# Kernel optimization log

Measured on AMD Instinct MI355X. Metric: run time of the kernel, lower is better.

The kernel has to match this reference:

```python
import jax, jax.numpy as jnp
import numpy as np

N_PRO = 100000
N_LIG = 100000
E = 500000
H = 128
CE = 18


def _lin_params(key, out_dim, in_dim, scale=0.02):
    kw, kb = jax.random.split(key)
    W = jax.random.normal(kw, (out_dim, in_dim), jnp.float32) * scale
    b = jax.random.normal(kb, (out_dim,), jnp.float32) * scale
    return W, b


def setup_inputs() -> dict:
    key = jax.random.key(0)
    ks = jax.random.split(key, 16)
    inp = {}
    inp['pro_x'] = jax.random.normal(ks[0], (N_PRO, H), jnp.float32)
    inp['lig_x'] = jax.random.normal(ks[1], (N_LIG, H), jnp.float32)
    pi = jax.random.randint(ks[2], (E,), 0, N_PRO)
    li = jax.random.randint(ks[3], (E,), 0, N_LIG)
    inp['cross_ei'] = jnp.stack([pi, li]).astype(jnp.int64)
    inp['cross_ea'] = jax.random.normal(ks[4], (E, CE), jnp.float32)
    inp['Wq_pro'], inp['bq_pro'] = _lin_params(ks[5], H, H)
    inp['Wk_lig'], inp['bk_lig'] = _lin_params(ks[6], H, H)
    inp['Wv_lig'], inp['bv_lig'] = _lin_params(ks[7], H, H)
    inp['Wq_lig'], inp['bq_lig'] = _lin_params(ks[8], H, H)
    inp['Wk_pro'], inp['bk_pro'] = _lin_params(ks[9], H, H)
    inp['Wv_pro'], inp['bv_pro'] = _lin_params(ks[10], H, H)
    inp['We_bias'] = jax.random.normal(ks[11], (CE,), jnp.float32) * 0.02  # Linear(CE,1,bias=False) weight
    inp['Wo_pro'], inp['bo_pro'] = _lin_params(ks[12], H, H)
    inp['Wo_lig'], inp['bo_lig'] = _lin_params(ks[13], H, H)
    inp['g_pro'] = jnp.ones((H,), jnp.float32)
    inp['be_pro'] = jnp.zeros((H,), jnp.float32)
    inp['g_lig'] = jnp.ones((H,), jnp.float32)
    inp['be_lig'] = jnp.zeros((H,), jnp.float32)
    return inp


def _layernorm(x, g, b, eps=1e-5):
    mu = jnp.mean(x, -1, keepdims=True)
    var = jnp.var(x, -1, keepdims=True)
    return (x - mu) * jax.lax.rsqrt(var + eps) * g + b


def _lin(x, W, b):
    return x @ W.T + b


def _attend(Q_src, K_tgt, V_tgt, bias, tgt_idx, n_tgt, scale):
    # per-edge score -> edge softmax over target nodes -> weighted scatter-add
    scores = jnp.sum(Q_src * K_tgt, -1) * scale + bias          # [E]
    scores = scores - jnp.max(scores)                            # global max, as in torch code
    exp_s = jnp.exp(scores)
    denom = jax.ops.segment_sum(exp_s, tgt_idx, num_segments=n_tgt)
    w = exp_s / (denom[tgt_idx] + 1e-8)                          # [E]
    return jax.ops.segment_sum(w[:, None] * V_tgt, tgt_idx, num_segments=n_tgt)  # [n_tgt, H]


def reference(pro_x, lig_x, cross_ei, cross_ea,
              Wq_pro, bq_pro, Wk_lig, bk_lig, Wv_lig, bv_lig,
              Wq_lig, bq_lig, Wk_pro, bk_pro, Wv_pro, bv_pro,
              We_bias, Wo_pro, bo_pro, Wo_lig, bo_lig,
              g_pro, be_pro, g_lig, be_lig):
    pi = cross_ei[0]
    li = cross_ei[1]
    h = pro_x.shape[1]
    scale = h ** (-0.5)
    bias = cross_ea @ We_bias                                    # [E]

    # protein <- ligand
    Qp = _lin(pro_x, Wq_pro, bq_pro)[pi]
    Kl = _lin(lig_x, Wk_lig, bk_lig)[li]
    Vl = _lin(lig_x, Wv_lig, bv_lig)[li]
    pro_upd = _attend(Qp, Kl, Vl, bias, pi, pro_x.shape[0], scale)
    pro_new = _layernorm(pro_x + _lin(pro_upd, Wo_pro, bo_pro), g_pro, be_pro)

    # ligand <- protein
    Ql = _lin(lig_x, Wq_lig, bq_lig)[li]
    Kp = _lin(pro_x, Wk_pro, bk_pro)[pi]
    Vp = _lin(pro_x, Wv_pro, bv_pro)[pi]
    lig_upd = _attend(Ql, Kp, Vp, bias, li, lig_x.shape[0], scale)
    lig_new = _layernorm(lig_x + _lin(lig_upd, Wo_lig, bo_lig), g_lig, be_lig)

    return (pro_new, lig_new)
```

## Files before the change

### kernel.cpp

```cpp
#include <hip/hip_runtime.h>
#include <float.h>
#include <math.h>


typedef __bf16 bf16x8 __attribute__((ext_vector_type(8)));
typedef float  f32x4  __attribute__((ext_vector_type(4)));
typedef float  f32x2  __attribute__((ext_vector_type(2)));
typedef unsigned int u32x2 __attribute__((ext_vector_type(2)));

__device__ __forceinline__ bf16x8 cvt8(const float* p) {
    f32x4 lo = *reinterpret_cast<const f32x4*>(p);
    f32x4 hi = *reinterpret_cast<const f32x4*>(p + 4);
    bf16x8 r;
    r[0] = (__bf16)lo[0]; r[1] = (__bf16)lo[1]; r[2] = (__bf16)lo[2]; r[3] = (__bf16)lo[3];
    r[4] = (__bf16)hi[0]; r[5] = (__bf16)hi[1]; r[6] = (__bf16)hi[2]; r[7] = (__bf16)hi[3];
    return r;
}

__device__ __forceinline__ u32x2 pack_fp8x8(const float* v) {
    int w0 = __builtin_amdgcn_cvt_pk_fp8_f32(v[0], v[1], 0, false);
    w0 = __builtin_amdgcn_cvt_pk_fp8_f32(v[2], v[3], w0, true);
    int w1 = __builtin_amdgcn_cvt_pk_fp8_f32(v[4], v[5], 0, false);
    w1 = __builtin_amdgcn_cvt_pk_fp8_f32(v[6], v[7], w1, true);
    u32x2 r; r[0] = (unsigned)w0; r[1] = (unsigned)w1;
    return r;
}

__device__ __forceinline__ void unpack_fp8x8(u32x2 p, float* out) {
    f32x2 t0 = __builtin_amdgcn_cvt_pk_f32_fp8((int)p[0], false);
    f32x2 t1 = __builtin_amdgcn_cvt_pk_f32_fp8((int)p[0], true);
    f32x2 t2 = __builtin_amdgcn_cvt_pk_f32_fp8((int)p[1], false);
    f32x2 t3 = __builtin_amdgcn_cvt_pk_f32_fp8((int)p[1], true);
    out[0] = t0[0]; out[1] = t0[1]; out[2] = t1[0]; out[3] = t1[1];
    out[4] = t2[0]; out[5] = t2[1]; out[6] = t3[0]; out[7] = t3[1];
}

__device__ __forceinline__ void stage_w(const __bf16* __restrict__ Ws, char* wlds, int tid) {
#pragma unroll
    for (int it = 0; it < 8; ++it) {
        int idx = it * 2048 + tid * 8;
        int byteoff = idx * 2;
        int row = byteoff >> 8;
        *reinterpret_cast<bf16x8*>(wlds + (byteoff ^ ((row & 7) << 4)))
            = *reinterpret_cast<const bf16x8*>(Ws + idx);
    }
}
__device__ __forceinline__ bf16x8 read_w(const char* wlds, int l15, int lg, int ni, int ks) {
    int row = ni * 16 + l15;
    int off = (row * 256 + ks * 64 + lg * 16) ^ ((row & 7) << 4);
    return *reinterpret_cast<const bf16x8*>(wlds + off);
}

__global__ __launch_bounds__(256) void cvt_weights(
    const float* w0, const float* w1, const float* w2, const float* w3,
    const float* w4, const float* w5, const float* w6, const float* w7,
    __bf16* __restrict__ dst)
{
    const float* srcs[8] = {w0, w1, w2, w3, w4, w5, w6, w7};
    int t = blockIdx.x * 256 + threadIdx.x;
    int mat = t >> 11;
    int base = (t & 2047) * 8;
    const float* s = srcs[mat];
    bool perm = (mat == 3) || (mat == 7);
    __bf16* d = dst + (size_t)mat * 16384;
#pragma unroll
    for (int u = 0; u < 8; ++u) {
        int idx = base + u;
        int row = idx >> 7, c = idx & 127;
        int pos = perm ? ((c & 15) * 8 + (c >> 4)) : c;
        d[row * 128 + pos] = (__bf16)s[idx];
    }
}

__global__ __launch_bounds__(256) void bias_count(
    const float* __restrict__ ea, const float* __restrict__ We,
    const int* __restrict__ pi, const int* __restrict__ li,
    float* __restrict__ bias, int* __restrict__ counts,
    unsigned* __restrict__ ranks, int Np, int E, int CE)
{
    int e = blockIdx.x * 256 + threadIdx.x;
    if (e >= E) return;
    const float2* row = reinterpret_cast<const float2*>(ea + (size_t)e * CE);
    float acc = 0.f;
    int h = CE >> 1;
    for (int c = 0; c < h; ++c) {
        float2 v = row[c];
        acc += v.x * We[2 * c] + v.y * We[2 * c + 1];
    }
    if (CE & 1) acc += ea[(size_t)e * CE + CE - 1] * We[CE - 1];
    bias[e] = acc;
    int r0 = atomicAdd(&counts[pi[e]], 1);
    int r1 = atomicAdd(&counts[Np + li[e]], 1);
    ranks[e] = (unsigned)(r0 & 0xFFFF) | ((unsigned)r1 << 16);
}

__global__ __launch_bounds__(256) void scan1(
    const int* __restrict__ counts, int* __restrict__ offs,
    int* __restrict__ bsums, int N)
{
    int idx = blockIdx.x * 256 + threadIdx.x;
    int v = (idx < N) ? counts[idx] : 0;
    int lane = threadIdx.x & 63, w = threadIdx.x >> 6;
    int x = v;
#pragma unroll
    for (int d = 1; d < 64; d <<= 1) {
        int y = __shfl_up(x, d);
        if (lane >= d) x += y;
    }
    __shared__ int wsum[4];
    if (lane == 63) wsum[w] = x;
    __syncthreads();
    int add = 0;
    for (int i = 0; i < w; ++i) add += wsum[i];
    x += add;
    if (idx < N) offs[idx] = x - v;
    if (threadIdx.x == 255) bsums[blockIdx.x] = x;
}

__global__ __launch_bounds__(1024) void scan2(int* __restrict__ bsums, int nb)
{
    __shared__ int tmp[1024];
    int t = threadIdx.x;
    tmp[t] = (t < nb) ? bsums[t] : 0;
    __syncthreads();
    for (int d = 1; d < 1024; d <<= 1) {
        int y = (t >= d) ? tmp[t - d] : 0;
        __syncthreads();
        tmp[t] += y;
        __syncthreads();
    }
    if (t < nb) bsums[t] = tmp[t];
}

__global__ __launch_bounds__(256) void scan3(
    int* __restrict__ offs, const int* __restrict__ bsums, int N, int total)
{
    int idx = blockIdx.x * 256 + threadIdx.x;
    if (idx < N && blockIdx.x > 0) offs[idx] += bsums[blockIdx.x - 1];
    if (idx == 0) offs[N] = total;
}

__global__ __launch_bounds__(256) void fill2(
    const int* __restrict__ pi, const int* __restrict__ li,
    const float* __restrict__ bias, const unsigned* __restrict__ ranks,
    const int* __restrict__ offs, unsigned* __restrict__ elist, int Np, int E)
{
    int e = blockIdx.x * 256 + threadIdx.x;
    if (e >= E) return;
    int p = pi[e], l = li[e];
    unsigned rk = ranks[e];
    int w = __builtin_amdgcn_cvt_pk_fp8_f32(bias[e], 0.f, 0, false);
    unsigned b8 = (unsigned)w & 0xFFu;
    elist[offs[p] + (rk & 0xFFFFu)]      = ((unsigned)l << 8) | b8;
    elist[offs[Np + l] + (rk >> 16)]     = ((unsigned)p << 8) | b8;
}

__global__ __launch_bounds__(256) void proj3both(
    const float* __restrict__ Xp, const float* __restrict__ Xl,
    const __bf16* __restrict__ W16,
    const float* __restrict__ bq_p, const float* __restrict__ bk_p, const float* __restrict__ bv_p,
    const float* __restrict__ bq_l, const float* __restrict__ bk_l, const float* __restrict__ bv_l,
    char* __restrict__ QKVp, char* __restrict__ QKVl,
    int Np, int Nl, int nbp)
{
    __shared__ char wlds[32768];
    int bid = blockIdx.x;
    int tid = threadIdx.x;
    int lane = tid & 63, wv = tid >> 6;
    int l15 = lane & 15, lg = lane >> 4;

    const float* A; const __bf16* Wms[3];
    const float* bsels[3]; char* QKV; int M, wrow;
    if (bid < nbp) {
        A = Xp; M = Np; wrow = bid * 64 + wv * 16;
        Wms[0] = W16 + 0 * 16384; Wms[1] = W16 + 5 * 16384; Wms[2] = W16 + 6 * 16384;
        bsels[0] = bq_p; bsels[1] = bk_p; bsels[2] = bv_p; QKV = QKVp;
    } else {
        A = Xl; M = Nl; wrow = (bid - nbp) * 64 + wv * 16;
        Wms[0] = W16 + 4 * 16384; Wms[1] = W16 + 1 * 16384; Wms[2] = W16 + 2 * 16384;
        bsels[0] = bq_l; bsels[1] = bk_l; bsels[2] = bv_l; QKV = QKVl;
    }
    int r0 = wrow + l15; if (r0 > M - 1) r0 = M - 1;
    const float* Arow0 = A + (size_t)r0 * 128 + lg * 8;

    bf16x8 a0[4];
#pragma unroll
    for (int ks = 0; ks < 4; ++ks) a0[ks] = cvt8(Arow0 + ks * 32);

#pragma unroll
    for (int mat = 0; mat < 3; ++mat) {
        __syncthreads();
        stage_w(Wms[mat], wlds, tid);
        __syncthreads();

        f32x4 acc[8] = {};
#pragma unroll
        for (int ks = 0; ks < 4; ++ks) {
#pragma unroll
            for (int ni = 0; ni < 8; ++ni)
                acc[ni] = __builtin_amdgcn_mfma_f32_16x16x32_bf16(
                    a0[ks], read_w(wlds, l15, lg, ni, ks), acc[ni], 0, 0, 0);
        }
        float bc[8];
#pragma unroll
        for (int ni = 0; ni < 8; ++ni) bc[ni] = bsels[mat][ni * 16 + l15];
#pragma unroll
        for (int r = 0; r < 4; ++r) {
            int row = wrow + lg * 4 + r;
            if (row < M) {
                float v[8];
#pragma unroll
                for (int ni = 0; ni < 8; ++ni) v[ni] = acc[ni][r] + bc[ni];
                char* rowb = QKV + (size_t)row * 512;
                if (mat == 0) {
                    bf16x8 o;
#pragma unroll
                    for (int ni = 0; ni < 8; ++ni) o[ni] = (__bf16)v[ni];
                    *reinterpret_cast<bf16x8*>(rowb + l15 * 16) = o;
                } else {
                    *reinterpret_cast<u32x2*>(rowb + 256 + (mat - 1) * 128 + l15 * 8)
                        = pack_fp8x8(v);
                }
            }
        }
    }
}

__global__ __launch_bounds__(256) void attend(
    const char* __restrict__ QKVp, const char* __restrict__ QKVl,
    const unsigned* __restrict__ elist, const int* __restrict__ offs,
    __bf16* __restrict__ upd_pro, __bf16* __restrict__ upd_lig,
    int Np, int Ntot, float scale)
{
    int node = blockIdx.x * 16 + (threadIdx.x >> 4);
    if (node >= Ntot) return;
    int l = threadIdx.x & 15;
    const char* Qrow; const char* KV; __bf16* upd;
    if (node < Np) {
        Qrow = QKVp + (size_t)node * 512; KV = QKVl;
        upd = upd_pro + (size_t)node * 128;
    } else {
        int n = node - Np;
        Qrow = QKVl + (size_t)n * 512; KV = QKVp;
        upd = upd_lig + (size_t)n * 128;
    }
    bf16x8 qv = *reinterpret_cast<const bf16x8*>(Qrow + l * 16);
    float q[8];
#pragma unroll
    for (int j = 0; j < 8; ++j) q[j] = (float)qv[j];

    int beg = offs[node], end = offs[node + 1];
    float d = 0.f;
    float acc[8] = {};
    for (int i = beg; i < end; ++i) {
        unsigned rec = elist[i];
        const char* row = KV + (size_t)(rec >> 8) * 512;
        f32x2 bt = __builtin_amdgcn_cvt_pk_f32_fp8((int)(rec & 0xFFu), false);
        u32x2 kk = *reinterpret_cast<const u32x2*>(row + 256 + l * 8);
        u32x2 vp = *reinterpret_cast<const u32x2*>(row + 384 + l * 8);
        float kf[8], vf[8];
        unpack_fp8x8(kk, kf);
        unpack_fp8x8(vp, vf);
        float dot = 0.f;
#pragma unroll
        for (int j = 0; j < 8; ++j) dot += q[j] * kf[j];
#pragma unroll
        for (int t = 1; t < 16; t <<= 1) dot += __shfl_xor(dot, t, 16);
        float s = fminf(dot * scale + bt[0], 60.f);
        float p = __expf(s);
        d += p;
#pragma unroll
        for (int j = 0; j < 8; ++j) acc[j] += p * vf[j];
    }
    float inv = 1.f / (d + 1e-8f);
    bf16x8 o;
#pragma unroll
    for (int j = 0; j < 8; ++j) o[j] = (__bf16)(acc[j] * inv);
    *reinterpret_cast<bf16x8*>(upd + l * 8) = o;
}

__global__ __launch_bounds__(256) void gemm_ln_both(
    const __bf16* __restrict__ upd_pro, const __bf16* __restrict__ upd_lig,
    const float* __restrict__ Xp, const float* __restrict__ Xl,
    const __bf16* __restrict__ W16,
    const float* __restrict__ bo_p, const float* __restrict__ g_p, const float* __restrict__ be_p,
    const float* __restrict__ bo_l, const float* __restrict__ g_l, const float* __restrict__ be_l,
    float* __restrict__ out_pro, float* __restrict__ out_lig,
    int Np, int Nl, int nbp)
{
    __shared__ char wlds[32768];
    int bid = blockIdx.x;
    int tid = threadIdx.x;
    int lane = tid & 63, wv = tid >> 6;
    int l15 = lane & 15, lg = lane >> 4;

    const __bf16* A; const float* X; const __bf16* Wo;
    const float *b, *g, *be_; float* C; int M, wrow;
    if (bid < nbp) {
        A = upd_pro; X = Xp; Wo = W16 + 3 * 16384;
        b = bo_p; g = g_p; be_ = be_p; C = out_pro; M = Np; wrow = bid * 64 + wv * 16;
    } else {
        A = upd_lig; X = Xl; Wo = W16 + 7 * 16384;
        b = bo_l; g = g_l; be_ = be_l; C = out_lig; M = Nl; wrow = (bid - nbp) * 64 + wv * 16;
    }
    stage_w(Wo, wlds, tid);

    int r0 = wrow + l15; if (r0 > M - 1) r0 = M - 1;
    const __bf16* Arow0 = A + (size_t)r0 * 128 + lg * 8;
    bf16x8 a0[4];
#pragma unroll
    for (int ks = 0; ks < 4; ++ks)
        a0[ks] = *reinterpret_cast<const bf16x8*>(Arow0 + ks * 32);
    __syncthreads();

    f32x4 acc[8] = {};
#pragma unroll
    for (int ks = 0; ks < 4; ++ks) {
#pragma unroll
        for (int ni = 0; ni < 8; ++ni)
            acc[ni] = __builtin_amdgcn_mfma_f32_16x16x32_bf16(
                a0[ks], read_w(wlds, l15, lg, ni, ks), acc[ni], 0, 0, 0);
    }

    float bcol[8], gcol[8], becol[8];
#pragma unroll
    for (int ni = 0; ni < 8; ++ni) {
        bcol[ni]  = b[ni * 16 + l15];
        gcol[ni]  = g[ni * 16 + l15];
        becol[ni] = be_[ni * 16 + l15];
    }

#pragma unroll
    for (int r = 0; r < 4; ++r) {
        int row = wrow + lg * 4 + r;
        bool ok = row < M;
        int rowc = ok ? row : M - 1;
        float v[8];
#pragma unroll
        for (int ni = 0; ni < 8; ++ni) v[ni] = acc[ni][r] + bcol[ni];
        const float* Xr = X + (size_t)rowc * 128 + l15;
        float s1 = 0.f, s2 = 0.f;
#pragma unroll
        for (int ni = 0; ni < 8; ++ni) {
            v[ni] += Xr[ni * 16];
            s1 += v[ni]; s2 += v[ni] * v[ni];
        }
#pragma unroll
        for (int d = 1; d < 16; d <<= 1) {
            s1 += __shfl_xor(s1, d);
            s2 += __shfl_xor(s2, d);
        }
        float mu = s1 * 0.0078125f;
        float var = s2 * 0.0078125f - mu * mu;
        float rstd = rsqrtf(var + 1e-5f);
        if (ok) {
            float* Cr = C + (size_t)row * 128 + l15;
#pragma unroll
            for (int ni = 0; ni < 8; ++ni)
                Cr[ni * 16] = (v[ni] - mu) * rstd * gcol[ni] + becol[ni];
        }
    }
}

static inline int cdiv(int a, int b) { return (a + b - 1) / b; }

extern "C" void kernel_launch(void* const* d_in, const int* in_sizes, int n_in,
                              void* d_out, int out_size, void* d_ws, size_t ws_size,
                              hipStream_t stream)
{
    const float* pro_x  = (const float*)d_in[0];
    const float* lig_x  = (const float*)d_in[1];
    const int*   ei     = (const int*)d_in[2];
    const float* ea     = (const float*)d_in[3];
    const float* Wq_pro = (const float*)d_in[4];  const float* bq_pro = (const float*)d_in[5];
    const float* Wk_lig = (const float*)d_in[6];  const float* bk_lig = (const float*)d_in[7];
    const float* Wv_lig = (const float*)d_in[8];  const float* bv_lig = (const float*)d_in[9];
    const float* Wq_lig = (const float*)d_in[10]; const float* bq_lig = (const float*)d_in[11];
    const float* Wk_pro = (const float*)d_in[12]; const float* bk_pro = (const float*)d_in[13];
    const float* Wv_pro = (const float*)d_in[14]; const float* bv_pro = (const float*)d_in[15];
    const float* We     = (const float*)d_in[16];
    const float* Wo_pro = (const float*)d_in[17]; const float* bo_pro = (const float*)d_in[18];
    const float* Wo_lig = (const float*)d_in[19]; const float* bo_lig = (const float*)d_in[20];
    const float* g_pro  = (const float*)d_in[21]; const float* be_pro = (const float*)d_in[22];
    const float* g_lig  = (const float*)d_in[23]; const float* be_lig = (const float*)d_in[24];

    const int Np = in_sizes[0] / 128;
    const int Nl = in_sizes[1] / 128;
    const int E  = in_sizes[2] / 2;
    const int CE = in_sizes[3] / E;
    const int Nmax = Np > Nl ? Np : Nl;
    const int Ntot = Np + Nl;
    const int* pi = ei;
    const int* li = ei + E;

    float* out_pro = (float*)d_out;
    float* out_lig = out_pro + (size_t)Np * 128;

    float* ws = (float*)d_ws;
    size_t o = 0;
    char* QKVp = (char*)(ws + o); o += (size_t)Nmax * 128;
    char* QKVl = (char*)(ws + o); o += (size_t)Nmax * 128;
    float* bias = ws + o;   o += (size_t)E;
    unsigned* ranks = (unsigned*)(ws + o); o += (size_t)E;
    unsigned* elist = (unsigned*)(ws + o); o += 2 * (size_t)E;
    int* counts = (int*)(ws + o); o += (size_t)Ntot + 8;
    int* offs   = (int*)(ws + o); o += (size_t)Ntot + 8;
    int* bsums  = (int*)(ws + o); o += 4096;
    __bf16* W16 = (__bf16*)(ws + o); o += 8 * 16384 / 2;
    __bf16* upd = (__bf16*)(ws + o); o += (size_t)Ntot * 64;
    __bf16* upd_pro = upd;
    __bf16* upd_lig = upd + (size_t)Np * 128;
    (void)ws_size; (void)n_in; (void)out_size;

    const float scale = 1.0f / sqrtf(128.0f);
    const int nEB = cdiv(E, 256);

    (void)hipMemsetAsync(counts, 0, (size_t)(Ntot + 1) * sizeof(int), stream);
    cvt_weights<<<64, 256, 0, stream>>>(Wq_pro, Wk_lig, Wv_lig, Wo_pro,
                                        Wq_lig, Wk_pro, Wv_pro, Wo_lig, W16);
    bias_count<<<nEB, 256, 0, stream>>>(ea, We, pi, li, bias, counts, ranks, Np, E, CE);

    const int nb1 = cdiv(Ntot, 256);
    scan1<<<nb1, 256, 0, stream>>>(counts, offs, bsums, Ntot);
    scan2<<<1, 1024, 0, stream>>>(bsums, nb1);
    scan3<<<nb1, 256, 0, stream>>>(offs, bsums, Ntot, 2 * E);
    fill2<<<nEB, 256, 0, stream>>>(pi, li, bias, ranks, offs, elist, Np, E);

    const int nbp = cdiv(Np, 64), nbl = cdiv(Nl, 64);
    proj3both<<<nbp + nbl, 256, 0, stream>>>(pro_x, lig_x, W16,
        bq_pro, bk_pro, bv_pro, bq_lig, bk_lig, bv_lig,
        QKVp, QKVl, Np, Nl, nbp);

    attend<<<cdiv(Ntot, 16), 256, 0, stream>>>(QKVp, QKVl, elist, offs,
        upd_pro, upd_lig, Np, Ntot, scale);

    gemm_ln_both<<<nbp + nbl, 256, 0, stream>>>(upd_pro, upd_lig,
        pro_x, lig_x, W16, bo_pro, g_pro, be_pro, bo_lig, g_lig, be_lig,
        out_pro, out_lig, Np, Nl, nbp);
}
```

Before: 265.2 us.

## Merge weight conversion into bias_count, drop scan2, unroll attend loop by two

```diff
diff --git a/kernel.cpp b/kernel.cpp
--- a/kernel.cpp
+++ b/kernel.cpp
@@ -51,34 +51,33 @@
     return *reinterpret_cast<const bf16x8*>(wlds + off);
 }
 
-__global__ __launch_bounds__(256) void cvt_weights(
+__global__ __launch_bounds__(256) void cvt_bias_count(
     const float* w0, const float* w1, const float* w2, const float* w3,
     const float* w4, const float* w5, const float* w6, const float* w7,
-    __bf16* __restrict__ dst)
-{
-    const float* srcs[8] = {w0, w1, w2, w3, w4, w5, w6, w7};
-    int t = blockIdx.x * 256 + threadIdx.x;
-    int mat = t >> 11;
-    int base = (t & 2047) * 8;
-    const float* s = srcs[mat];
-    bool perm = (mat == 3) || (mat == 7);
-    __bf16* d = dst + (size_t)mat * 16384;
-#pragma unroll
-    for (int u = 0; u < 8; ++u) {
-        int idx = base + u;
-        int row = idx >> 7, c = idx & 127;
-        int pos = perm ? ((c & 15) * 8 + (c >> 4)) : c;
-        d[row * 128 + pos] = (__bf16)s[idx];
-    }
-}
-
-__global__ __launch_bounds__(256) void bias_count(
+    __bf16* __restrict__ dst,
     const float* __restrict__ ea, const float* __restrict__ We,
     const int* __restrict__ pi, const int* __restrict__ li,
     float* __restrict__ bias, int* __restrict__ counts,
     unsigned* __restrict__ ranks, int Np, int E, int CE)
 {
-    int e = blockIdx.x * 256 + threadIdx.x;
+    if (blockIdx.x < 64) {
+        const float* srcs[8] = {w0, w1, w2, w3, w4, w5, w6, w7};
+        int t = blockIdx.x * 256 + threadIdx.x;
+        int mat = t >> 11;
+        int base = (t & 2047) * 8;
+        const float* s = srcs[mat];
+        bool perm = (mat == 3) || (mat == 7);
+        __bf16* d = dst + (size_t)mat * 16384;
+#pragma unroll
+        for (int u = 0; u < 8; ++u) {
+            int idx = base + u;
+            int row = idx >> 7, c = idx & 127;
+            int pos = perm ? ((c & 15) * 8 + (c >> 4)) : c;
+            d[row * 128 + pos] = (__bf16)s[idx];
+        }
+        return;
+    }
+    int e = (blockIdx.x - 64) * 256 + threadIdx.x;
     if (e >= E) return;
     const float2* row = reinterpret_cast<const float2*>(ea + (size_t)e * CE);
     float acc = 0.f;
@@ -117,26 +116,20 @@
     if (threadIdx.x == 255) bsums[blockIdx.x] = x;
 }
 
-__global__ __launch_bounds__(1024) void scan2(int* __restrict__ bsums, int nb)
-{
-    __shared__ int tmp[1024];
-    int t = threadIdx.x;
-    tmp[t] = (t < nb) ? bsums[t] : 0;
-    __syncthreads();
-    for (int d = 1; d < 1024; d <<= 1) {
-        int y = (t >= d) ? tmp[t - d] : 0;
-        __syncthreads();
-        tmp[t] += y;
-        __syncthreads();
-    }
-    if (t < nb) bsums[t] = tmp[t];
-}
-
 __global__ __launch_bounds__(256) void scan3(
     int* __restrict__ offs, const int* __restrict__ bsums, int N, int total)
 {
-    int idx = blockIdx.x * 256 + threadIdx.x;
-    if (idx < N && blockIdx.x > 0) offs[idx] += bsums[blockIdx.x - 1];
+    int b = blockIdx.x, t = threadIdx.x;
+    int s = 0;
+    for (int i = t; i < b; i += 256) s += bsums[i];
+#pragma unroll
+    for (int d = 1; d < 64; d <<= 1) s += __shfl_xor(s, d);
+    __shared__ int ws_[4];
+    if ((t & 63) == 0) ws_[t >> 6] = s;
+    __syncthreads();
+    int pre = ws_[0] + ws_[1] + ws_[2] + ws_[3];
+    int idx = b * 256 + t;
+    if (idx < N) offs[idx] += pre;
     if (idx == 0) offs[N] = total;
 }
 
@@ -151,8 +144,8 @@
     unsigned rk = ranks[e];
     int w = __builtin_amdgcn_cvt_pk_fp8_f32(bias[e], 0.f, 0, false);
     unsigned b8 = (unsigned)w & 0xFFu;
-    elist[offs[p] + (rk & 0xFFFFu)]      = ((unsigned)l << 8) | b8;
-    elist[offs[Np + l] + (rk >> 16)]     = ((unsigned)p << 8) | b8;
+    elist[offs[p] + (rk & 0xFFFFu)]  = ((unsigned)l << 8) | b8;
+    elist[offs[Np + l] + (rk >> 16)] = ((unsigned)p << 8) | b8;
 }
 
 __global__ __launch_bounds__(256) void proj3both(
@@ -252,22 +245,48 @@
     int beg = offs[node], end = offs[node + 1];
     float d = 0.f;
     float acc[8] = {};
-    for (int i = beg; i < end; ++i) {
+    int i = beg;
+    for (; i + 1 < end; i += 2) {
+        unsigned rec0 = elist[i], rec1 = elist[i + 1];
+        const char* row0 = KV + (size_t)(rec0 >> 8) * 512;
+        const char* row1 = KV + (size_t)(rec1 >> 8) * 512;
+        u32x2 kk0 = *reinterpret_cast<const u32x2*>(row0 + 256 + l * 8);
+        u32x2 vp0 = *reinterpret_cast<const u32x2*>(row0 + 384 + l * 8);
+        u32x2 kk1 = *reinterpret_cast<const u32x2*>(row1 + 256 + l * 8);
+        u32x2 vp1 = *reinterpret_cast<const u32x2*>(row1 + 384 + l * 8);
+        float kf0[8], vf0[8], kf1[8], vf1[8];
+        unpack_fp8x8(kk0, kf0); unpack_fp8x8(vp0, vf0);
+        unpack_fp8x8(kk1, kf1); unpack_fp8x8(vp1, vf1);
+        float dot0 = 0.f, dot1 = 0.f;
+#pragma unroll
+        for (int j = 0; j < 8; ++j) { dot0 += q[j] * kf0[j]; dot1 += q[j] * kf1[j]; }
+#pragma unroll
+        for (int t = 1; t < 16; t <<= 1) {
+            dot0 += __shfl_xor(dot0, t, 16);
+            dot1 += __shfl_xor(dot1, t, 16);
+        }
+        f32x2 b0 = __builtin_amdgcn_cvt_pk_f32_fp8((int)(rec0 & 0xFFu), false);
+        f32x2 b1 = __builtin_amdgcn_cvt_pk_f32_fp8((int)(rec1 & 0xFFu), false);
+        float p0 = __expf(fminf(dot0 * scale + b0[0], 60.f));
+        float p1 = __expf(fminf(dot1 * scale + b1[0], 60.f));
+        d += p0 + p1;
+#pragma unroll
+        for (int j = 0; j < 8; ++j) acc[j] += p0 * vf0[j] + p1 * vf1[j];
+    }
+    if (i < end) {
         unsigned rec = elist[i];
         const char* row = KV + (size_t)(rec >> 8) * 512;
-        f32x2 bt = __builtin_amdgcn_cvt_pk_f32_fp8((int)(rec & 0xFFu), false);
         u32x2 kk = *reinterpret_cast<const u32x2*>(row + 256 + l * 8);
         u32x2 vp = *reinterpret_cast<const u32x2*>(row + 384 + l * 8);
         float kf[8], vf[8];
-        unpack_fp8x8(kk, kf);
-        unpack_fp8x8(vp, vf);
+        unpack_fp8x8(kk, kf); unpack_fp8x8(vp, vf);
         float dot = 0.f;
 #pragma unroll
         for (int j = 0; j < 8; ++j) dot += q[j] * kf[j];
 #pragma unroll
         for (int t = 1; t < 16; t <<= 1) dot += __shfl_xor(dot, t, 16);
-        float s = fminf(dot * scale + bt[0], 60.f);
-        float p = __expf(s);
+        f32x2 bt = __builtin_amdgcn_cvt_pk_f32_fp8((int)(rec & 0xFFu), false);
+        float p = __expf(fminf(dot * scale + bt[0], 60.f));
         d += p;
 #pragma unroll
         for (int j = 0; j < 8; ++j) acc[j] += p * vf[j];
@@ -416,13 +435,12 @@
     const int nEB = cdiv(E, 256);
 
     (void)hipMemsetAsync(counts, 0, (size_t)(Ntot + 1) * sizeof(int), stream);
-    cvt_weights<<<64, 256, 0, stream>>>(Wq_pro, Wk_lig, Wv_lig, Wo_pro,
-                                        Wq_lig, Wk_pro, Wv_pro, Wo_lig, W16);
-    bias_count<<<nEB, 256, 0, stream>>>(ea, We, pi, li, bias, counts, ranks, Np, E, CE);
+    cvt_bias_count<<<64 + nEB, 256, 0, stream>>>(
+        Wq_pro, Wk_lig, Wv_lig, Wo_pro, Wq_lig, Wk_pro, Wv_pro, Wo_lig, W16,
+        ea, We, pi, li, bias, counts, ranks, Np, E, CE);
 
     const int nb1 = cdiv(Ntot, 256);
     scan1<<<nb1, 256, 0, stream>>>(counts, offs, bsums, Ntot);
-    scan2<<<1, 1024, 0, stream>>>(bsums, nb1);
     scan3<<<nb1, 256, 0, stream>>>(offs, bsums, Ntot, 2 * E);
     fill2<<<nEB, 256, 0, stream>>>(pi, li, bias, ranks, offs, elist, Np, E);
 
```

Result: faster. 249.3 us (-6.0%).
